# Kernel optimization log

Hardware: AMD Instinct MI355X
Metric: run time of the kernel (lower is better)

## Reference

```python
import jax, jax.numpy as jnp
import numpy as np
import math

B, L, D, H, NT, T, NLAYERS = 64, 128, 512, 8, 10000, 65536, 2
DH = D // H
FF = 2 * D
EPS = 1e-5


def setup_inputs() -> dict:
    key = jax.random.key(0)
    ks = jax.random.split(key, 20)
    item_ids = jax.random.randint(ks[0], (T,), 0, NT, dtype=jnp.int32)
    seg_ids = jnp.sort(jax.random.randint(ks[1], (T,), 0, B * L, dtype=jnp.int32))
    pad_mask = jnp.zeros((B, L), dtype=bool)
    future_mask = jnp.where(jnp.triu(jnp.ones((L, L), dtype=bool), k=1), -1e9, 0.0).astype(jnp.float32)

    s = 0.02
    emb = (jax.random.normal(ks[2], (NT + 1, D), jnp.float32) * s).at[NT].set(0.0)  # padding_idx row is zero
    Wqkv = jax.random.normal(ks[3], (NLAYERS, 3 * D, D), jnp.float32) * s
    bqkv = jnp.zeros((NLAYERS, 3 * D), jnp.float32)
    Wo = jax.random.normal(ks[4], (NLAYERS, D, D), jnp.float32) * s
    bo = jnp.zeros((NLAYERS, D), jnp.float32)
    W1 = jax.random.normal(ks[5], (NLAYERS, FF, D), jnp.float32) * s
    b1 = jnp.zeros((NLAYERS, FF), jnp.float32)
    W2 = jax.random.normal(ks[6], (NLAYERS, D, FF), jnp.float32) * s
    b2 = jnp.zeros((NLAYERS, D), jnp.float32)
    ln1_s = jnp.ones((NLAYERS, D), jnp.float32)
    ln1_b = jnp.zeros((NLAYERS, D), jnp.float32)
    ln2_s = jnp.ones((NLAYERS, D), jnp.float32)
    ln2_b = jnp.zeros((NLAYERS, D), jnp.float32)
    Wout = jax.random.normal(ks[7], (NT, D), jnp.float32) * s
    bout = jnp.zeros((NT,), jnp.float32)
    return dict(item_ids=item_ids, seg_ids=seg_ids, pad_mask=pad_mask, future_mask=future_mask,
                max_len=L, emb=emb, Wqkv=Wqkv, bqkv=bqkv, Wo=Wo, bo=bo, W1=W1, b1=b1, W2=W2, b2=b2,
                ln1_s=ln1_s, ln1_b=ln1_b, ln2_s=ln2_s, ln2_b=ln2_b, Wout=Wout, bout=bout)


def _layernorm(x, s, b):
    m = jnp.mean(x, axis=-1, keepdims=True)
    v = jnp.mean(jnp.square(x - m), axis=-1, keepdims=True)
    return (x - m) * jax.lax.rsqrt(v + EPS) * s + b


def _pos_encoding(maxlen, d):
    den = jnp.exp(-jnp.arange(0, d, 2, dtype=jnp.float32) * (math.log(10000.0) / d))
    pos = jnp.arange(maxlen, dtype=jnp.float32)[:, None]
    pe = jnp.zeros((maxlen, d), jnp.float32)
    pe = pe.at[:, 0::2].set(jnp.sin(pos * den))
    pe = pe.at[:, 1::2].set(jnp.cos(pos * den))
    return pe


def reference(item_ids, seg_ids, pad_mask, future_mask, max_len, emb,
              Wqkv, bqkv, Wo, bo, W1, b1, W2, b2, ln1_s, ln1_b, ln2_s, ln2_b, Wout, bout):
    # fused gather + segment-mean (replaces the per-user Python loops)
    counts = jax.ops.segment_sum(jnp.ones((T,), jnp.float32), seg_ids, num_segments=B * max_len)
    sums = jax.ops.segment_sum(emb[item_ids], seg_ids, num_segments=B * max_len)  # [B*L, D]
    means = jnp.where(counts[:, None] > 0, sums / jnp.maximum(counts, 1.0)[:, None], 0.0)
    x = means.reshape(B, max_len, D) + _pos_encoding(max_len, D)

    key_mask = jnp.where(pad_mask[:, None, None, :], -1e9, 0.0)  # [B,1,1,L]
    scale = 1.0 / math.sqrt(DH)
    for i in range(NLAYERS):
        qkv = x @ Wqkv[i].T + bqkv[i]                         # [B,L,3D]
        q, k, v = jnp.split(qkv, 3, axis=-1)
        q = q.reshape(B, max_len, H, DH)
        k = k.reshape(B, max_len, H, DH)
        v = v.reshape(B, max_len, H, DH)
        scores = jnp.einsum('bqhd,bkhd->bhqk', q, k) * scale + future_mask + key_mask
        attn = jax.nn.softmax(scores, axis=-1)
        o = jnp.einsum('bhqk,bkhd->bqhd', attn, v).reshape(B, max_len, D)
        o = o @ Wo[i].T + bo[i]
        x = _layernorm(x + o, ln1_s[i], ln1_b[i])              # post-norm
        ff = jax.nn.relu(x @ W1[i].T + b1[i]) @ W2[i].T + b2[i]
        x = _layernorm(x + ff, ln2_s[i], ln2_b[i])
    return x @ Wout.T + bout  # [B, L, num_types]
```

## Files before the change

### kernel.cpp

```cpp
#include <hip/hip_runtime.h>

#define T_TOTAL 65536
#define SEQ 128
#define DMODEL 512
#define DHEAD 64
#define NTYPES 10000
#define ROWS 8192
#define NOUT_PAD 10240

typedef float floatx4 __attribute__((ext_vector_type(4)));
typedef short shortx8 __attribute__((ext_vector_type(8)));

#define GLOAD_LDS(gp, lp) __builtin_amdgcn_global_load_lds( \
    (const __attribute__((address_space(1))) void*)(gp),    \
    (__attribute__((address_space(3))) void*)(lp), 16, 0, 0)

#define MFMA_BF16 __builtin_amdgcn_mfma_f32_16x16x32_bf16

__device__ __forceinline__ unsigned short f2bf(float f) {
  union { float f; unsigned u; } v; v.f = f;
  unsigned u = v.u + 0x7fffu + ((v.u >> 16) & 1u);
  return (unsigned short)(u >> 16);
}

__device__ __forceinline__ void phase_barrier() {
  __builtin_amdgcn_sched_barrier(0);
  __builtin_amdgcn_s_barrier();
  __builtin_amdgcn_sched_barrier(0);
}

__global__ __launch_bounds__(256) void convert_all_kernel(
    const float* __restrict__ Wqkv, const float* __restrict__ Wo,
    const float* __restrict__ W1, const float* __restrict__ W2,
    const float* __restrict__ Wout,
    unsigned short* __restrict__ wqkv_b, unsigned short* __restrict__ wo_b,
    unsigned short* __restrict__ w1_b, unsigned short* __restrict__ w2_b,
    unsigned short* __restrict__ wout_b) {
  const long Q0 = 1572864L / 4;
  const long Q1 = Q0 + 524288L / 4;
  const long Q2 = Q1 + 1048576L / 4;
  const long Q3 = Q2 + 1048576L / 4;
  const long Q4 = Q3 + 5242880L / 4;
  const long stride = 2048L * 256;
  for (long q = (long)blockIdx.x * 256 + threadIdx.x; q < Q4; q += stride) {
    const float* src; unsigned short* dst; long i; bool guard = false;
    if (q < Q0)      { src = Wqkv; dst = wqkv_b; i = q; }
    else if (q < Q1) { src = Wo;   dst = wo_b;   i = q - Q0; }
    else if (q < Q2) { src = W1;   dst = w1_b;   i = q - Q1; }
    else if (q < Q3) { src = W2;   dst = w2_b;   i = q - Q2; }
    else             { src = Wout; dst = wout_b; i = q - Q3; guard = true; }
    long e = i * 4;
    float4 v = make_float4(0.f, 0.f, 0.f, 0.f);
    if (!guard || e < 5120000L) v = *(const float4*)(src + e);
    ushort4 o;
    o.x = f2bf(v.x); o.y = f2bf(v.y); o.z = f2bf(v.z); o.w = f2bf(v.w);
    *(ushort4*)(dst + e) = o;
  }
}

__global__ __launch_bounds__(128) void seg_mean_kernel(
    const int* __restrict__ item_ids, const int* __restrict__ seg_ids,
    const float* __restrict__ emb, float* __restrict__ x_f,
    unsigned short* __restrict__ x_b) {
  int s = blockIdx.x;
  int lo = 0, hi = T_TOTAL;
  while (lo < hi) { int mid = (lo + hi) >> 1; if (seg_ids[mid] < s) lo = mid + 1; else hi = mid; }
  int start = lo;
  hi = T_TOTAL;
  while (lo < hi) { int mid = (lo + hi) >> 1; if (seg_ids[mid] <= s) lo = mid + 1; else hi = mid; }
  int end = lo;
  int c = threadIdx.x << 2;
  float4 acc = make_float4(0.f, 0.f, 0.f, 0.f);
  for (int j = start; j < end; ++j) {
    const float* e = emb + (long)item_ids[j] * DMODEL + c;
    float4 v = *(const float4*)e;
    acc.x += v.x; acc.y += v.y; acc.z += v.z; acc.w += v.w;
  }
  int cnt = end - start;
  float inv = cnt > 0 ? 1.0f / (float)cnt : 0.0f;
  float mv[4] = {acc.x * inv, acc.y * inv, acc.z * inv, acc.w * inv};
  int l = s & (SEQ - 1);
  const float klog = 0.017988946039015984f;
  long base = (long)s * DMODEL + c;
#pragma unroll
  for (int t = 0; t < 4; ++t) {
    int col = c + t;
    float den = expf(-(float)(col & ~1) * klog);
    float ang = (float)l * den;
    float pe = (col & 1) ? cosf(ang) : sinf(ang);
    float val = mv[t] + pe;
    x_f[base + t] = val;
    x_b[base + t] = f2bf(val);
  }
}

__global__ __launch_bounds__(256) void gemm_bt_kernel(
    const unsigned short* __restrict__ A,
    const unsigned short* __restrict__ B,
    const float* __restrict__ bias,
    float* __restrict__ Cf,
    unsigned short* __restrict__ Cb,
    int K, int Nreal, int ldC, int relu) {
  __shared__ unsigned short As[128 * 32];
  __shared__ unsigned short Bs[128 * 32];
  const int tid = threadIdx.x;
  const int lane = tid & 63;
  const int wave = tid >> 6;
  const int wm = (wave >> 1) << 6;
  const int wn = (wave & 1) << 6;
  const int l16 = lane & 15;
  const int quad = lane >> 4;
  const long rowA0 = (long)blockIdx.x * 128;
  const long rowB0 = (long)blockIdx.y * 128;

  floatx4 acc[4][4] = {};

  const int rowOff = tid >> 2;
  const int kOff = (tid & 3) << 3;
  const unsigned short* gA = A + (rowA0 + rowOff) * (long)K + kOff;
  const unsigned short* gB = B + (rowB0 + rowOff) * (long)K + kOff;
  unsigned short* lA = As + tid * 8;
  unsigned short* lB = Bs + tid * 8;

  for (int k0 = 0; k0 < K; k0 += 32) {
    __syncthreads();
    GLOAD_LDS(gA + k0, lA);
    GLOAD_LDS(gA + 64 * (long)K + k0, lA + 2048);
    GLOAD_LDS(gB + k0, lB);
    GLOAD_LDS(gB + 64 * (long)K + k0, lB + 2048);
    __syncthreads();
    shortx8 af[4], bfr[4];
#pragma unroll
    for (int i = 0; i < 4; ++i)
      af[i] = *(const shortx8*)(As + (wm + i * 16 + l16) * 32 + quad * 8);
#pragma unroll
    for (int j = 0; j < 4; ++j)
      bfr[j] = *(const shortx8*)(Bs + (wn + j * 16 + l16) * 32 + quad * 8);
#pragma unroll
    for (int i = 0; i < 4; ++i)
#pragma unroll
      for (int j = 0; j < 4; ++j)
        acc[i][j] = MFMA_BF16(af[i], bfr[j], acc[i][j], 0, 0, 0);
  }

#pragma unroll
  for (int i = 0; i < 4; ++i) {
    int row = (int)rowA0 + wm + i * 16 + quad * 4;
#pragma unroll
    for (int j = 0; j < 4; ++j) {
      int col = (int)rowB0 + wn + j * 16 + l16;
      if (col < Nreal) {
        float bv = bias ? bias[col] : 0.0f;
#pragma unroll
        for (int r = 0; r < 4; ++r) {
          float v = acc[i][j][r] + bv;
          if (relu) v = fmaxf(v, 0.0f);
          long off = (long)(row + r) * ldC + col;
          if (Cf) Cf[off] = v;
          if (Cb) Cb[off] = f2bf(v);
        }
      }
    }
  }
}

__device__ __forceinline__ void frag_read(const unsigned short* __restrict__ base,
                                          int R, int quad, shortx8& f0, shortx8& f1) {
  int pc = quad ^ (R & 7);
  const unsigned short* p = base + R * 64;
  f0 = *(const shortx8*)(p + pc * 8);
  f1 = *(const shortx8*)(p + (pc ^ 4) * 8);
}

__global__ __launch_bounds__(512, 2) void gemm256_kernel(
    const unsigned short* __restrict__ A,
    const unsigned short* __restrict__ B,
    const float* __restrict__ bias,
    float* __restrict__ Cf,
    unsigned short* __restrict__ Cb,
    int K, int Nreal, int ldC, int relu) {
  __shared__ unsigned short As[2][256 * 64];
  __shared__ unsigned short Bs[2][256 * 64];
  const int tid = threadIdx.x;
  const int lane = tid & 63;
  const int wave = tid >> 6;
  const int wm = wave >> 2;
  const int wn = wave & 3;
  const int l16 = lane & 15;
  const int quad = lane >> 4;
  const long rowA0 = (long)blockIdx.x * 256;
  const long rowB0 = (long)blockIdx.y * 256;

  floatx4 acc[8][4] = {};

  const int srow = tid >> 3;
  const int scol = (((tid & 7) ^ ((tid >> 3) & 7)) << 3);
  const unsigned short* gA = A + (rowA0 + srow) * (long)K + scol;
  const unsigned short* gB = B + (rowB0 + srow) * (long)K + scol;
  const int loff = tid * 8;
  const long rstep = 64 * (long)K;

#pragma unroll
  for (int is = 0; is < 4; ++is) {
    GLOAD_LDS(gA + is * rstep, &As[0][is * 4096 + loff]);
    GLOAD_LDS(gB + is * rstep, &Bs[0][is * 4096 + loff]);
  }
  asm volatile("s_waitcnt vmcnt(0)" ::: "memory");
  phase_barrier();

  const int KT = K >> 6;
  for (int kt = 0; kt < KT; ++kt) {
    const int cur = kt & 1;
    const unsigned short* Ab = As[cur];
    const unsigned short* Bb = Bs[cur];
    unsigned short* An = As[cur ^ 1];
    unsigned short* Bn = Bs[cur ^ 1];
    const bool stage = (kt + 1) < KT;
    const unsigned short* gAn = gA + (long)(kt + 1) * 64;
    const unsigned short* gBn = gB + (long)(kt + 1) * 64;

    shortx8 af[4][2], bf[4][2];

#pragma unroll
    for (int m = 0; m < 4; ++m)
      frag_read(Ab, wm * 128 + m * 16 + l16, quad, af[m][0], af[m][1]);
#pragma unroll
    for (int n = 0; n < 2; ++n)
      frag_read(Bb, wn * 64 + n * 16 + l16, quad, bf[n][0], bf[n][1]);
    if (stage) {
      GLOAD_LDS(gAn, An + loff);
      GLOAD_LDS(gAn + rstep, An + 4096 + loff);
      GLOAD_LDS(gAn + 2 * rstep, An + 8192 + loff);
      GLOAD_LDS(gAn + 3 * rstep, An + 12288 + loff);
    }
    phase_barrier();
    __builtin_amdgcn_s_setprio(1);
#pragma unroll
    for (int m = 0; m < 4; ++m)
#pragma unroll
      for (int n = 0; n < 2; ++n) {
        acc[m][n] = MFMA_BF16(af[m][0], bf[n][0], acc[m][n], 0, 0, 0);
        acc[m][n] = MFMA_BF16(af[m][1], bf[n][1], acc[m][n], 0, 0, 0);
      }
    __builtin_amdgcn_s_setprio(0);
    phase_barrier();

#pragma unroll
    for (int n = 2; n < 4; ++n)
      frag_read(Bb, wn * 64 + n * 16 + l16, quad, bf[n][0], bf[n][1]);
    if (stage) {
      GLOAD_LDS(gBn, Bn + loff);
      GLOAD_LDS(gBn + rstep, Bn + 4096 + loff);
      GLOAD_LDS(gBn + 2 * rstep, Bn + 8192 + loff);
      GLOAD_LDS(gBn + 3 * rstep, Bn + 12288 + loff);
    }
    phase_barrier();
    __builtin_amdgcn_s_setprio(1);
#pragma unroll
    for (int m = 0; m < 4; ++m)
#pragma unroll
      for (int n = 2; n < 4; ++n) {
        acc[m][n] = MFMA_BF16(af[m][0], bf[n][0], acc[m][n], 0, 0, 0);
        acc[m][n] = MFMA_BF16(af[m][1], bf[n][1], acc[m][n], 0, 0, 0);
      }
    __builtin_amdgcn_s_setprio(0);
    phase_barrier();

#pragma unroll
    for (int m = 0; m < 4; ++m)
      frag_read(Ab, wm * 128 + 64 + m * 16 + l16, quad, af[m][0], af[m][1]);
    phase_barrier();
    __builtin_amdgcn_s_setprio(1);
#pragma unroll
    for (int m = 0; m < 4; ++m)
#pragma unroll
      for (int n = 0; n < 2; ++n) {
        acc[4 + m][n] = MFMA_BF16(af[m][0], bf[n][0], acc[4 + m][n], 0, 0, 0);
        acc[4 + m][n] = MFMA_BF16(af[m][1], bf[n][1], acc[4 + m][n], 0, 0, 0);
      }
    __builtin_amdgcn_s_setprio(0);
    phase_barrier();

    __builtin_amdgcn_s_setprio(1);
#pragma unroll
    for (int m = 0; m < 4; ++m)
#pragma unroll
      for (int n = 2; n < 4; ++n) {
        acc[4 + m][n] = MFMA_BF16(af[m][0], bf[n][0], acc[4 + m][n], 0, 0, 0);
        acc[4 + m][n] = MFMA_BF16(af[m][1], bf[n][1], acc[4 + m][n], 0, 0, 0);
      }
    __builtin_amdgcn_s_setprio(0);
    asm volatile("s_waitcnt vmcnt(0)" ::: "memory");
    phase_barrier();
  }

#pragma unroll
  for (int m = 0; m < 8; ++m) {
    int row = (int)rowA0 + wm * 128 + m * 16 + quad * 4;
#pragma unroll
    for (int n = 0; n < 4; ++n) {
      int col = (int)rowB0 + wn * 64 + n * 16 + l16;
      if (col < Nreal) {
        float bv = bias ? bias[col] : 0.0f;
#pragma unroll
        for (int r = 0; r < 4; ++r) {
          float v = acc[m][n][r] + bv;
          if (relu) v = fmaxf(v, 0.0f);
          long off = (long)(row + r) * ldC + col;
          if (Cf) Cf[off] = v;
          if (Cb) Cb[off] = f2bf(v);
        }
      }
    }
  }
}

__global__ __launch_bounds__(256) void attn_kernel(
    const float* __restrict__ qkv,
    unsigned short* __restrict__ o_b) {
  __shared__ float Ks[SEQ * DHEAD];
  __shared__ float Vs[SEQ * DHEAD];
  __shared__ float Ds[SEQ];
  int b = blockIdx.x >> 3, h = blockIdx.x & 7;
  const float* base = qkv + (long)b * SEQ * 1536;
  int hoff = h * DHEAD;
  for (int idx4 = threadIdx.x; idx4 < SEQ * DHEAD / 4; idx4 += 256) {
    int l = idx4 >> 4;
    int c4 = (idx4 & 15) << 2;
    *(float4*)(Ks + l * 64 + c4) = *(const float4*)(base + l * 1536 + 512 + hoff + c4);
    *(float4*)(Vs + l * 64 + c4) = *(const float4*)(base + l * 1536 + 1024 + hoff + c4);
  }
  __syncthreads();
  int l = threadIdx.x & 127;
  int half = threadIdx.x >> 7;
  float q[DHEAD];
#pragma unroll
  for (int c4 = 0; c4 < 16; ++c4)
    *(float4*)(q + c4 * 4) = *(const float4*)(base + l * 1536 + hoff + c4 * 4);
  float o[DHEAD];
#pragma unroll
  for (int c = 0; c < DHEAD; ++c) o[c] = 0.f;
  float denom = 0.f;
  for (int j = half; j <= l; j += 2) {
    const float* kr = Ks + j * DHEAD;
    float s0 = 0.f, s1 = 0.f, s2 = 0.f, s3 = 0.f;
#pragma unroll
    for (int c = 0; c < DHEAD; c += 4) {
      s0 += q[c] * kr[c];         s1 += q[c + 1] * kr[c + 1];
      s2 += q[c + 2] * kr[c + 2]; s3 += q[c + 3] * kr[c + 3];
    }
    float p = __expf(((s0 + s1) + (s2 + s3)) * 0.125f);
    denom += p;
    const float* vr = Vs + j * DHEAD;
#pragma unroll
    for (int c = 0; c < DHEAD; ++c) o[c] += p * vr[c];
  }
  __syncthreads();
  if (half) {
    float* os = Ks + l * DHEAD;
#pragma unroll
    for (int c = 0; c < DHEAD; ++c) os[c] = o[c];
    Ds[l] = denom;
  }
  __syncthreads();
  if (!half) {
    float dtot = denom + Ds[l];
    float inv = 1.0f / dtot;
    const float* os = Ks + l * DHEAD;
    unsigned short* dst = o_b + ((long)b * SEQ + l) * DMODEL + hoff;
#pragma unroll
    for (int c0 = 0; c0 < DHEAD; c0 += 8) {
      shortx8 ov;
#pragma unroll
      for (int k = 0; k < 8; ++k)
        ov[k] = (short)f2bf((o[c0 + k] + os[c0 + k]) * inv);
      *(shortx8*)(dst + c0) = ov;
    }
  }
}

__global__ __launch_bounds__(256) void add_ln_kernel(
    const float* __restrict__ x_in, const float* __restrict__ delta,
    const float* __restrict__ gamma, const float* __restrict__ beta,
    float* __restrict__ x_f, unsigned short* __restrict__ x_b) {
  int row = blockIdx.x;
  int tid = threadIdx.x;
  long base = (long)row * DMODEL;
  int c = tid * 2;
  float2 xv = *(const float2*)(x_in + base + c);
  float2 dv = *(const float2*)(delta + base + c);
  float a = xv.x + dv.x, b = xv.y + dv.y;
  float s = a + b;
  float sq = a * a + b * b;
#pragma unroll
  for (int off = 32; off > 0; off >>= 1) {
    s += __shfl_down(s, off, 64);
    sq += __shfl_down(sq, off, 64);
  }
  __shared__ float red[8];
  __shared__ float mean_s, rstd_s;
  int wv = tid >> 6, ln = tid & 63;
  if (ln == 0) { red[wv] = s; red[4 + wv] = sq; }
  __syncthreads();
  if (tid == 0) {
    float S = red[0] + red[1] + red[2] + red[3];
    float SQ = red[4] + red[5] + red[6] + red[7];
    float mean = S * (1.0f / 512.0f);
    float var = SQ * (1.0f / 512.0f) - mean * mean;
    mean_s = mean;
    rstd_s = rsqrtf(var + 1e-5f);
  }
  __syncthreads();
  float mean = mean_s, rstd = rstd_s;
  float o0 = (a - mean) * rstd * gamma[c] + beta[c];
  float o1 = (b - mean) * rstd * gamma[c + 1] + beta[c + 1];
  x_f[base + c] = o0;
  x_f[base + c + 1] = o1;
  x_b[base + c] = f2bf(o0);
  x_b[base + c + 1] = f2bf(o1);
}

extern "C" void kernel_launch(void* const* d_in, const int* in_sizes, int n_in,
                              void* d_out, int out_size, void* d_ws, size_t ws_size,
                              hipStream_t stream) {
  const int* item_ids = (const int*)d_in[0];
  const int* seg_ids = (const int*)d_in[1];
  const float* emb  = (const float*)d_in[5];
  const float* Wqkv = (const float*)d_in[6];
  const float* bqkv = (const float*)d_in[7];
  const float* Wo   = (const float*)d_in[8];
  const float* bo   = (const float*)d_in[9];
  const float* W1   = (const float*)d_in[10];
  const float* b1   = (const float*)d_in[11];
  const float* W2   = (const float*)d_in[12];
  const float* b2   = (const float*)d_in[13];
  const float* ln1s = (const float*)d_in[14];
  const float* ln1b = (const float*)d_in[15];
  const float* ln2s = (const float*)d_in[16];
  const float* ln2b = (const float*)d_in[17];
  const float* Wout = (const float*)d_in[18];
  const float* bout = (const float*)d_in[19];
  float* out = (float*)d_out;

  char* ws = (char*)d_ws;
  size_t off = 0;
  auto alloc = [&](size_t bytes) {
    void* p = ws + off;
    off += (bytes + 255) & ~(size_t)255;
    return p;
  };
  float* x_f  = (float*)alloc((size_t)ROWS * 512 * 4);
  unsigned short* x_b = (unsigned short*)alloc((size_t)ROWS * 512 * 2);
  float* qkv_f = (float*)alloc((size_t)ROWS * 1536 * 4);
  unsigned short* o_b = (unsigned short*)alloc((size_t)ROWS * 512 * 2);
  float* tmp_f = (float*)alloc((size_t)ROWS * 512 * 4);
  unsigned short* h_b = (unsigned short*)alloc((size_t)ROWS * 1024 * 2);
  unsigned short* wqkv_b = (unsigned short*)alloc((size_t)2 * 1536 * 512 * 2);
  unsigned short* wo_b = (unsigned short*)alloc((size_t)2 * 512 * 512 * 2);
  unsigned short* w1_b = (unsigned short*)alloc((size_t)2 * 1024 * 512 * 2);
  unsigned short* w2_b = (unsigned short*)alloc((size_t)2 * 512 * 1024 * 2);
  unsigned short* wout_b = (unsigned short*)alloc((size_t)NOUT_PAD * 512 * 2);

  convert_all_kernel<<<2048, 256, 0, stream>>>(
      Wqkv, Wo, W1, W2, Wout, wqkv_b, wo_b, w1_b, w2_b, wout_b);

  seg_mean_kernel<<<ROWS, 128, 0, stream>>>(item_ids, seg_ids, emb, x_f, x_b);

  for (int i = 0; i < 2; ++i) {
    gemm256_kernel<<<dim3(32, 6), 512, 0, stream>>>(
        x_b, wqkv_b + (long)i * 1536 * 512, bqkv + i * 1536,
        qkv_f, nullptr, 512, 1536, 1536, 0);
    attn_kernel<<<512, 256, 0, stream>>>(qkv_f, o_b);
    gemm_bt_kernel<<<dim3(64, 4), 256, 0, stream>>>(
        o_b, wo_b + (long)i * 512 * 512, bo + i * 512,
        tmp_f, nullptr, 512, 512, 512, 0);
    add_ln_kernel<<<ROWS, 256, 0, stream>>>(x_f, tmp_f, ln1s + i * 512, ln1b + i * 512, x_f, x_b);
    gemm_bt_kernel<<<dim3(64, 8), 256, 0, stream>>>(
        x_b, w1_b + (long)i * 1024 * 512, b1 + i * 1024,
        nullptr, h_b, 512, 1024, 1024, 1);
    gemm_bt_kernel<<<dim3(64, 4), 256, 0, stream>>>(
        h_b, w2_b + (long)i * 512 * 1024, b2 + i * 512,
        tmp_f, nullptr, 1024, 512, 512, 0);
    add_ln_kernel<<<ROWS, 256, 0, stream>>>(x_f, tmp_f, ln2s + i * 512, ln2b + i * 512, x_f, x_b);
  }

  gemm256_kernel<<<dim3(32, 40), 512, 0, stream>>>(
      x_b, wout_b, bout, out, nullptr, 512, NTYPES, NTYPES, 0);
}
```

Measured before the change: 899.4 us.

## Fuse residual LayerNorm into GEMM epilogue, precompute segment starts, swizzle tiles

Adds a gemm_ln kernel in which each 512-thread block computes a full 64x512 output row tile. It applies bias, residual add and LayerNorm in the epilogue, which removes the separate add_ln kernels and the tmp_f round trip. The prep kernel now also builds a segment start table, so seg_mean no longer runs two binary searches per segment. gemm256 gets a grid swizzle for better L2 reuse. The new fused GEMM uses a simple single-buffered 32-wide K loop with two syncs per step and only 128 blocks, which may underutilize the GPU compared with the tuned gemm_bt path.

Result: no change. 902.0 us (+0.3%).

```diff
diff --git a/kernel.cpp b/kernel.cpp
--- a/kernel.cpp
+++ b/kernel.cpp
@@ -29,20 +29,29 @@
   __builtin_amdgcn_sched_barrier(0);
 }
 
-__global__ __launch_bounds__(256) void convert_all_kernel(
+__global__ __launch_bounds__(256) void prep_kernel(
     const float* __restrict__ Wqkv, const float* __restrict__ Wo,
     const float* __restrict__ W1, const float* __restrict__ W2,
     const float* __restrict__ Wout,
     unsigned short* __restrict__ wqkv_b, unsigned short* __restrict__ wo_b,
     unsigned short* __restrict__ w1_b, unsigned short* __restrict__ w2_b,
-    unsigned short* __restrict__ wout_b) {
+    unsigned short* __restrict__ wout_b,
+    const int* __restrict__ seg_ids, int* __restrict__ starts) {
+  long gid = (long)blockIdx.x * 256 + threadIdx.x;
+  if (gid < T_TOTAL) {
+    int cur = seg_ids[gid];
+    int prev = (gid == 0) ? -1 : seg_ids[gid - 1];
+    for (int s = prev + 1; s <= cur; ++s) starts[s] = (int)gid;
+    if (gid == T_TOTAL - 1)
+      for (int s = cur + 1; s <= ROWS; ++s) starts[s] = T_TOTAL;
+  }
   const long Q0 = 1572864L / 4;
   const long Q1 = Q0 + 524288L / 4;
   const long Q2 = Q1 + 1048576L / 4;
   const long Q3 = Q2 + 1048576L / 4;
   const long Q4 = Q3 + 5242880L / 4;
   const long stride = 2048L * 256;
-  for (long q = (long)blockIdx.x * 256 + threadIdx.x; q < Q4; q += stride) {
+  for (long q = gid; q < Q4; q += stride) {
     const float* src; unsigned short* dst; long i; bool guard = false;
     if (q < Q0)      { src = Wqkv; dst = wqkv_b; i = q; }
     else if (q < Q1) { src = Wo;   dst = wo_b;   i = q - Q0; }
@@ -59,16 +68,11 @@
 }
 
 __global__ __launch_bounds__(128) void seg_mean_kernel(
-    const int* __restrict__ item_ids, const int* __restrict__ seg_ids,
+    const int* __restrict__ item_ids, const int* __restrict__ starts,
     const float* __restrict__ emb, float* __restrict__ x_f,
     unsigned short* __restrict__ x_b) {
   int s = blockIdx.x;
-  int lo = 0, hi = T_TOTAL;
-  while (lo < hi) { int mid = (lo + hi) >> 1; if (seg_ids[mid] < s) lo = mid + 1; else hi = mid; }
-  int start = lo;
-  hi = T_TOTAL;
-  while (lo < hi) { int mid = (lo + hi) >> 1; if (seg_ids[mid] <= s) lo = mid + 1; else hi = mid; }
-  int end = lo;
+  int start = starts[s], end = starts[s + 1];
   int c = threadIdx.x << 2;
   float4 acc = make_float4(0.f, 0.f, 0.f, 0.f);
   for (int j = start; j < end; ++j) {
@@ -164,6 +168,121 @@
   }
 }
 
+__global__ __launch_bounds__(512) void gemm_ln_kernel(
+    const unsigned short* __restrict__ A,
+    const unsigned short* __restrict__ W,
+    const float* __restrict__ bias,
+    const float* __restrict__ gamma, const float* __restrict__ beta,
+    float* __restrict__ x_f,
+    unsigned short* __restrict__ x_b,
+    int K) {
+  __shared__ unsigned short As[64 * 32];
+  __shared__ unsigned short Bs[512 * 32];
+  __shared__ float redS[64][4];
+  __shared__ float redQ[64][4];
+  __shared__ float meanr[64], rstdr[64];
+  const int tid = threadIdx.x;
+  const int lane = tid & 63;
+  const int wave = tid >> 6;
+  const int wr = wave >> 2;
+  const int wc = wave & 3;
+  const int l16 = lane & 15;
+  const int quad = lane >> 4;
+  const long row0 = (long)blockIdx.x * 64;
+
+  floatx4 acc[2][8] = {};
+
+  const unsigned short* gA = A + (row0 + (tid >> 2)) * (long)K + ((tid & 3) << 3);
+  const unsigned short* gW = W + (long)(tid >> 2) * K + ((tid & 3) << 3);
+  const long rstepW = 128 * (long)K;
+  unsigned short* lA = As + tid * 8;
+  unsigned short* lB = Bs + tid * 8;
+
+  for (int k0 = 0; k0 < K; k0 += 32) {
+    __syncthreads();
+    if (tid < 256) GLOAD_LDS(gA + k0, lA);
+#pragma unroll
+    for (int is = 0; is < 4; ++is)
+      GLOAD_LDS(gW + is * rstepW + k0, lB + is * 4096);
+    __syncthreads();
+    shortx8 af[2], bf[8];
+#pragma unroll
+    for (int i = 0; i < 2; ++i)
+      af[i] = *(const shortx8*)(As + (wr * 32 + i * 16 + l16) * 32 + quad * 8);
+#pragma unroll
+    for (int j = 0; j < 8; ++j)
+      bf[j] = *(const shortx8*)(Bs + (wc * 128 + j * 16 + l16) * 32 + quad * 8);
+#pragma unroll
+    for (int i = 0; i < 2; ++i)
+#pragma unroll
+      for (int j = 0; j < 8; ++j)
+        acc[i][j] = MFMA_BF16(af[i], bf[j], acc[i][j], 0, 0, 0);
+  }
+
+  float e[2][8][4];
+  float sP[2][4] = {{0.f, 0.f, 0.f, 0.f}, {0.f, 0.f, 0.f, 0.f}};
+  float qP[2][4] = {{0.f, 0.f, 0.f, 0.f}, {0.f, 0.f, 0.f, 0.f}};
+#pragma unroll
+  for (int i = 0; i < 2; ++i)
+#pragma unroll
+    for (int r = 0; r < 4; ++r) {
+      int rloc = wr * 32 + i * 16 + quad * 4 + r;
+      long rbase = (row0 + rloc) * DMODEL;
+#pragma unroll
+      for (int j = 0; j < 8; ++j) {
+        int col = wc * 128 + j * 16 + l16;
+        float v = acc[i][j][r] + bias[col] + x_f[rbase + col];
+        e[i][j][r] = v;
+        sP[i][r] += v;
+        qP[i][r] += v * v;
+      }
+    }
+#pragma unroll
+  for (int m = 1; m < 16; m <<= 1)
+#pragma unroll
+    for (int i = 0; i < 2; ++i)
+#pragma unroll
+      for (int r = 0; r < 4; ++r) {
+        sP[i][r] += __shfl_xor(sP[i][r], m, 64);
+        qP[i][r] += __shfl_xor(qP[i][r], m, 64);
+      }
+  if (l16 == 0) {
+#pragma unroll
+    for (int i = 0; i < 2; ++i)
+#pragma unroll
+      for (int r = 0; r < 4; ++r) {
+        int rloc = wr * 32 + i * 16 + quad * 4 + r;
+        redS[rloc][wc] = sP[i][r];
+        redQ[rloc][wc] = qP[i][r];
+      }
+  }
+  __syncthreads();
+  if (tid < 64) {
+    float S = redS[tid][0] + redS[tid][1] + redS[tid][2] + redS[tid][3];
+    float Q = redQ[tid][0] + redQ[tid][1] + redQ[tid][2] + redQ[tid][3];
+    float mean = S * (1.0f / 512.0f);
+    float var = Q * (1.0f / 512.0f) - mean * mean;
+    meanr[tid] = mean;
+    rstdr[tid] = rsqrtf(var + 1e-5f);
+  }
+  __syncthreads();
+#pragma unroll
+  for (int i = 0; i < 2; ++i)
+#pragma unroll
+    for (int r = 0; r < 4; ++r) {
+      int rloc = wr * 32 + i * 16 + quad * 4 + r;
+      long rbase = (row0 + rloc) * DMODEL;
+      float mean = meanr[rloc], rstd = rstdr[rloc];
+#pragma unroll
+      for (int j = 0; j < 8; ++j) {
+        int col = wc * 128 + j * 16 + l16;
+        float o = (e[i][j][r] - mean) * rstd * gamma[col] + beta[col];
+        x_f[rbase + col] = o;
+        x_b[rbase + col] = f2bf(o);
+      }
+    }
+}
+
 __device__ __forceinline__ void frag_read(const unsigned short* __restrict__ base,
                                           int R, int quad, shortx8& f0, shortx8& f1) {
   int pc = quad ^ (R & 7);
@@ -188,8 +307,12 @@
   const int wn = wave & 3;
   const int l16 = lane & 15;
   const int quad = lane >> 4;
-  const long rowA0 = (long)blockIdx.x * 256;
-  const long rowB0 = (long)blockIdx.y * 256;
+  const int nwgx = gridDim.x;
+  const int flat = blockIdx.y * nwgx + blockIdx.x;
+  const int cpx = (nwgx * gridDim.y) >> 3;
+  const int swz = (flat & 7) * cpx + (flat >> 3);
+  const long rowA0 = (long)(swz % nwgx) * 256;
+  const long rowB0 = (long)(swz / nwgx) * 256;
 
   floatx4 acc[8][4] = {};
 
@@ -377,47 +500,6 @@
       *(shortx8*)(dst + c0) = ov;
     }
   }
-}
-
-__global__ __launch_bounds__(256) void add_ln_kernel(
-    const float* __restrict__ x_in, const float* __restrict__ delta,
-    const float* __restrict__ gamma, const float* __restrict__ beta,
-    float* __restrict__ x_f, unsigned short* __restrict__ x_b) {
-  int row = blockIdx.x;
-  int tid = threadIdx.x;
-  long base = (long)row * DMODEL;
-  int c = tid * 2;
-  float2 xv = *(const float2*)(x_in + base + c);
-  float2 dv = *(const float2*)(delta + base + c);
-  float a = xv.x + dv.x, b = xv.y + dv.y;
-  float s = a + b;
-  float sq = a * a + b * b;
-#pragma unroll
-  for (int off = 32; off > 0; off >>= 1) {
-    s += __shfl_down(s, off, 64);
-    sq += __shfl_down(sq, off, 64);
-  }
-  __shared__ float red[8];
-  __shared__ float mean_s, rstd_s;
-  int wv = tid >> 6, ln = tid & 63;
-  if (ln == 0) { red[wv] = s; red[4 + wv] = sq; }
-  __syncthreads();
-  if (tid == 0) {
-    float S = red[0] + red[1] + red[2] + red[3];
-    float SQ = red[4] + red[5] + red[6] + red[7];
-    float mean = S * (1.0f / 512.0f);
-    float var = SQ * (1.0f / 512.0f) - mean * mean;
-    mean_s = mean;
-    rstd_s = rsqrtf(var + 1e-5f);
-  }
-  __syncthreads();
-  float mean = mean_s, rstd = rstd_s;
-  float o0 = (a - mean) * rstd * gamma[c] + beta[c];
-  float o1 = (b - mean) * rstd * gamma[c + 1] + beta[c + 1];
-  x_f[base + c] = o0;
-  x_f[base + c + 1] = o1;
-  x_b[base + c] = f2bf(o0);
-  x_b[base + c + 1] = f2bf(o1);
 }
 
 extern "C" void kernel_launch(void* const* d_in, const int* in_sizes, int n_in,
@@ -453,35 +535,33 @@
   unsigned short* x_b = (unsigned short*)alloc((size_t)ROWS * 512 * 2);
   float* qkv_f = (float*)alloc((size_t)ROWS * 1536 * 4);
   unsigned short* o_b = (unsigned short*)alloc((size_t)ROWS * 512 * 2);
-  float* tmp_f = (float*)alloc((size_t)ROWS * 512 * 4);
   unsigned short* h_b = (unsigned short*)alloc((size_t)ROWS * 1024 * 2);
   unsigned short* wqkv_b = (unsigned short*)alloc((size_t)2 * 1536 * 512 * 2);
   unsigned short* wo_b = (unsigned short*)alloc((size_t)2 * 512 * 512 * 2);
   unsigned short* w1_b = (unsigned short*)alloc((size_t)2 * 1024 * 512 * 2);
   unsigned short* w2_b = (unsigned short*)alloc((size_t)2 * 512 * 1024 * 2);
   unsigned short* wout_b = (unsigned short*)alloc((size_t)NOUT_PAD * 512 * 2);
-
-  convert_all_kernel<<<2048, 256, 0, stream>>>(
-      Wqkv, Wo, W1, W2, Wout, wqkv_b, wo_b, w1_b, w2_b, wout_b);
-
-  seg_mean_kernel<<<ROWS, 128, 0, stream>>>(item_ids, seg_ids, emb, x_f, x_b);
+  int* starts = (int*)alloc((size_t)(ROWS + 1) * 4);
+
+  prep_kernel<<<2048, 256, 0, stream>>>(
+      Wqkv, Wo, W1, W2, Wout, wqkv_b, wo_b, w1_b, w2_b, wout_b, seg_ids, starts);
+
+  seg_mean_kernel<<<ROWS, 128, 0, stream>>>(item_ids, starts, emb, x_f, x_b);
 
   for (int i = 0; i < 2; ++i) {
     gemm256_kernel<<<dim3(32, 6), 512, 0, stream>>>(
         x_b, wqkv_b + (long)i * 1536 * 512, bqkv + i * 1536,
         qkv_f, nullptr, 512, 1536, 1536, 0);
     attn_kernel<<<512, 256, 0, stream>>>(qkv_f, o_b);
-    gemm_bt_kernel<<<dim3(64, 4), 256, 0, stream>>>(
+    gemm_ln_kernel<<<128, 512, 0, stream>>>(
         o_b, wo_b + (long)i * 512 * 512, bo + i * 512,
-        tmp_f, nullptr, 512, 512, 512, 0);
-    add_ln_kernel<<<ROWS, 256, 0, stream>>>(x_f, tmp_f, ln1s + i * 512, ln1b + i * 512, x_f, x_b);
+        ln1s + i * 512, ln1b + i * 512, x_f, x_b, 512);
     gemm_bt_kernel<<<dim3(64, 8), 256, 0, stream>>>(
         x_b, w1_b + (long)i * 1024 * 512, b1 + i * 1024,
         nullptr, h_b, 512, 1024, 1024, 1);
-    gemm_bt_kernel<<<dim3(64, 4), 256, 0, stream>>>(
+    gemm_ln_kernel<<<128, 512, 0, stream>>>(
         h_b, w2_b + (long)i * 512 * 1024, b2 + i * 512,
-        tmp_f, nullptr, 1024, 512, 512, 0);
-    add_ln_kernel<<<ROWS, 256, 0, stream>>>(x_f, tmp_f, ln2s + i * 512, ln2b + i * 512, x_f, x_b);
+        ln2s + i * 512, ln2b + i * 512, x_f, x_b, 1024);
   }
 
   gemm256_kernel<<<dim3(32, 40), 512, 0, stream>>>(
```
